# Kernel tuning notes

Hardware: AMD Instinct MI355X
Metric: run time of the kernel (lower is better)

## Reference

```python
import jax, jax.numpy as jnp
from jax import lax
import numpy as np

B = 16
E, NH, FF, L = 768, 12, 3072, 8
D = E // NH  # 64, per-head dim
PATCH_DIM = 16 * 16 * 16  # 4096


def setup_inputs() -> dict:
    key = jax.random.key(0)
    ks = jax.random.split(key, 16)
    s = 0.02
    def n(k, shape):
        return jax.random.normal(k, shape, dtype=jnp.float32) * s
    return {
        "x": jax.random.normal(ks[0], (B, 512, 512, 3), dtype=jnp.float32),
        "conv1_w": n(ks[1], (3, 3, 3, 16)), "conv1_b": jnp.zeros((16,), jnp.float32),
        "conv2_w": n(ks[2], (3, 3, 16, 16)), "conv2_b": jnp.zeros((16,), jnp.float32),
        "proj_w": n(ks[3], (PATCH_DIM, E)), "proj_b": jnp.zeros((E,), jnp.float32),
        "Wq": n(ks[4], (L, E, E)), "bq": jnp.zeros((L, E), jnp.float32),
        "Wk": n(ks[5], (L, E, E)), "bk": jnp.zeros((L, E), jnp.float32),
        "Wv": n(ks[6], (L, E, E)), "bv": jnp.zeros((L, E), jnp.float32),
        "Wo": n(ks[7], (L, E, E)), "bo": jnp.zeros((L, E), jnp.float32),
        "W1": n(ks[8], (L, E, FF)), "b1": jnp.zeros((L, FF), jnp.float32),
        "W2": n(ks[9], (L, FF, E)), "b2": jnp.zeros((L, E), jnp.float32),
        "ln1_g": jnp.ones((L, E), jnp.float32), "ln1_b": jnp.zeros((L, E), jnp.float32),
        "ln2_g": jnp.ones((L, E), jnp.float32), "ln2_b": jnp.zeros((L, E), jnp.float32),
        "head_w": n(ks[10], (E, 1)), "head_b": jnp.zeros((1,), jnp.float32),
    }


def _ln(x, g, b, eps=1e-6):
    m = jnp.mean(x, axis=-1, keepdims=True)
    v = jnp.var(x, axis=-1, keepdims=True)
    return (x - m) * lax.rsqrt(v + eps) * g + b


def _forward(x, conv1_w, conv1_b, conv2_w, conv2_b, proj_w, proj_b,
             Wq, bq, Wk, bk, Wv, bv, Wo, bo, W1, b1, W2, b2,
             ln1_g, ln1_b, ln2_g, ln2_b, head_w, head_b):
    dn = ('NHWC', 'HWIO', 'NHWC')
    h = jax.nn.relu(lax.conv_general_dilated(x, conv1_w, (1, 1), 'VALID', dimension_numbers=dn) + conv1_b)
    h = lax.reduce_window(h, -jnp.inf, lax.max, (1, 2, 2, 1), (1, 2, 2, 1), 'VALID')  # (B,255,255,16)
    h = jax.nn.relu(lax.conv_general_dilated(h, conv2_w, (1, 1), 'VALID', dimension_numbers=dn) + conv2_b)
    h = lax.reduce_window(h, -jnp.inf, lax.max, (1, 2, 2, 1), (1, 2, 2, 1), 'VALID')  # (B,126,126,16)
    # tf.image.extract_patches 16x16 stride 16 SAME: pad 126 -> 128 (1 before, 1 after)
    h = jnp.pad(h, ((0, 0), (1, 1), (1, 1), (0, 0)))
    Bc = h.shape[0]
    patches = h.reshape(Bc, 8, 16, 8, 16, 16).transpose(0, 1, 3, 2, 4, 5).reshape(Bc, 64, PATCH_DIM)
    t = patches @ proj_w + proj_b  # (B,64,768)
    scale = 1.0 / jnp.sqrt(jnp.float32(D))  # tf code scales by sqrt(per-head key dim)
    for i in range(L):
        q = (t @ Wq[i] + bq[i]).reshape(Bc, -1, NH, D).transpose(0, 2, 1, 3)
        k = (t @ Wk[i] + bk[i]).reshape(Bc, -1, NH, D).transpose(0, 2, 1, 3)
        v = (t @ Wv[i] + bv[i]).reshape(Bc, -1, NH, D).transpose(0, 2, 1, 3)
        w = jax.nn.softmax(jnp.einsum('bhqd,bhkd->bhqk', q, k) * scale, axis=-1)
        a = jnp.einsum('bhqk,bhkd->bhqd', w, v)  # (B,H,S,D)
        # FAITHFUL to original: reshape (B,H,S,D) -> (B,S,E) directly (no transpose back)
        a = a.reshape(Bc, -1, E)
        a = a @ Wo[i] + bo[i]
        o1 = _ln(t + a, ln1_g[i], ln1_b[i])
        f = jax.nn.relu(o1 @ W1[i] + b1[i]) @ W2[i] + b2[i]
        t = _ln(o1 + f, ln2_g[i], ln2_b[i])
    pooled = jnp.mean(t, axis=1)  # GlobalAveragePooling1D
    return jax.nn.sigmoid(pooled @ head_w + head_b)


def reference(x, conv1_w, conv1_b, conv2_w, conv2_b, proj_w, proj_b,
              Wq, bq, Wk, bk, Wv, bv, Wo, bo, W1, b1, W2, b2,
              ln1_g, ln1_b, ln2_g, ln2_b, head_w, head_b):
    return _forward(x, conv1_w, conv1_b, conv2_w, conv2_b, proj_w, proj_b,
                    Wq, bq, Wk, bk, Wv, bv, Wo, bo, W1, b1, W2, b2,
                    ln1_g, ln1_b, ln2_g, ln2_b, head_w, head_b)
```

## Files before the change

### kernel.cpp

```cpp
#include <hip/hip_runtime.h>
#include <hip/hip_bf16.h>
#include <cstdint>
#include <cstddef>

typedef __bf16 bf16;
typedef __attribute__((ext_vector_type(8))) __bf16 bf16x8;
typedef __attribute__((ext_vector_type(4))) float f32x4;

__global__ __launch_bounds__(256) void wtrans(const float* __restrict__ src,
    bf16* __restrict__ dst, int K, int N) {
  __shared__ float tile[32][33];
  int l = blockIdx.z;
  src += (size_t)l * K * N; dst += (size_t)l * K * N;
  int n0 = blockIdx.x * 32, k0 = blockIdx.y * 32;
  int tx = threadIdx.x & 31, ty = threadIdx.x >> 5;
#pragma unroll
  for (int i = 0; i < 4; i++) {
    int k = ty + i * 8;
    tile[k][tx] = src[(size_t)(k0 + k) * N + n0 + tx];
  }
  __syncthreads();
#pragma unroll
  for (int i = 0; i < 4; i++) {
    int n = ty + i * 8;
    dst[(size_t)(n0 + n) * K + k0 + tx] = (bf16)tile[tx][n];
  }
}

__global__ __launch_bounds__(256) void conv1_pool(const float* __restrict__ x,
    const float* __restrict__ w, const float* __restrict__ bias,
    bf16* __restrict__ out) {
  __shared__ float ws[432];
  __shared__ float bs[16];
  int t = threadIdx.x;
  for (int i = t; i < 432; i += 256) ws[i] = w[i];
  if (t < 16) bs[t] = bias[t];
  __syncthreads();
  int idx = blockIdx.x * 256 + t;
  if (idx >= 16 * 255 * 255) return;
  int xo = idx % 255; int tmp = idx / 255; int yo = tmp % 255; int b = tmp / 255;
  float best[16];
#pragma unroll
  for (int c = 0; c < 16; c++) best[c] = 0.f;
#pragma unroll
  for (int py = 0; py < 2; py++)
#pragma unroll
  for (int px = 0; px < 2; px++) {
    float acc[16];
#pragma unroll
    for (int c = 0; c < 16; c++) acc[c] = bs[c];
    int iy0 = yo * 2 + py, ix0 = xo * 2 + px;
    for (int ky = 0; ky < 3; ky++)
    for (int kx = 0; kx < 3; kx++) {
      const float* xp = x + ((size_t)(b * 512 + iy0 + ky) * 512 + (ix0 + kx)) * 3;
      float v0 = xp[0], v1 = xp[1], v2 = xp[2];
      const float* wp = &ws[((ky * 3 + kx) * 3) * 16];
#pragma unroll
      for (int c = 0; c < 16; c++) acc[c] = fmaf(v0, wp[c], acc[c]);
#pragma unroll
      for (int c = 0; c < 16; c++) acc[c] = fmaf(v1, wp[16 + c], acc[c]);
#pragma unroll
      for (int c = 0; c < 16; c++) acc[c] = fmaf(v2, wp[32 + c], acc[c]);
    }
#pragma unroll
    for (int c = 0; c < 16; c++) best[c] = fmaxf(best[c], acc[c]);
  }
  bf16* op = out + (size_t)idx * 16;
#pragma unroll
  for (int c = 0; c < 16; c++) op[c] = (bf16)best[c];
}

__global__ __launch_bounds__(256) void conv2_mfma(const bf16* __restrict__ in,
    const float* __restrict__ w, const float* __restrict__ bias,
    bf16* __restrict__ patches) {
  __shared__ alignas(16) bf16 xlo[1156 * 8];
  __shared__ alignas(16) bf16 xhi[1156 * 8];
  __shared__ float ws[2304];
  int t = threadIdx.x;
  int tx = blockIdx.x, ty = blockIdx.y, b = blockIdx.z;
  for (int i = t; i < 2304; i += 256) ws[i] = w[i];
  int r0 = 32 * ty - 2, c0 = 32 * tx - 2;
  for (int i = t; i < 1156; i += 256) {
    int rr = i / 34, cc = i % 34;
    int gr = min(max(r0 + rr, 0), 254), gc = min(max(c0 + cc, 0), 254);
    const bf16* ip = in + ((size_t)(b * 255 + gr) * 255 + gc) * 16;
    *(uint4*)&xlo[i * 8] = *(const uint4*)ip;
    *(uint4*)&xhi[i * 8] = *(const uint4*)(ip + 8);
  }
  __syncthreads();
  int lane = t & 63, wave = t >> 6;
  int lr = lane & 15, lq = lane >> 4;
  int tapsel = lq >> 1;
  int ci0 = (lq & 1) * 8;
  bf16x8 bfrag[5];
  int koff[5];
#pragma unroll
  for (int c2 = 0; c2 < 5; c2++) {
    int tap = 2 * c2 + tapsel;
    bf16x8 v;
#pragma unroll
    for (int j = 0; j < 8; j++)
      v[j] = (tap < 9) ? (bf16)ws[tap * 256 + (ci0 + j) * 16 + lr] : (bf16)0.f;
    bfrag[c2] = v;
    int tc = min(tap, 8);
    koff[c2] = (tc / 3) * 34 + (tc % 3);
  }
  const bf16* plane = (lq & 1) ? xhi : xlo;
  float bco = bias[lr];
  bf16* pout = patches + ((size_t)(b * 64 + ty * 8 + tx) * 4096);
#pragma unroll
  for (int yy = 0; yy < 4; yy++) {
    int Y = wave * 4 + yy;
    int yp = ty * 16 + Y;
    bool padrow = (yp == 0 || yp == 127);
#pragma unroll
    for (int hx = 0; hx < 2; hx++) {
      f32x4 a0 = {0.f, 0.f, 0.f, 0.f}, a1 = {0.f, 0.f, 0.f, 0.f};
      int base0 = (2 * Y) * 34 + hx * 16 + lr;
      int base1 = base0 + 34;
#pragma unroll
      for (int c2 = 0; c2 < 5; c2++) {
        bf16x8 f0 = *(const bf16x8*)&plane[(base0 + koff[c2]) * 8];
        a0 = __builtin_amdgcn_mfma_f32_16x16x32_bf16(f0, bfrag[c2], a0, 0, 0, 0);
      }
#pragma unroll
      for (int c2 = 0; c2 < 5; c2++) {
        bf16x8 f1 = *(const bf16x8*)&plane[(base1 + koff[c2]) * 8];
        a1 = __builtin_amdgcn_mfma_f32_16x16x32_bf16(f1, bfrag[c2], a1, 0, 0, 0);
      }
      float m0 = fmaxf(fmaxf(a0[0], a0[1]), fmaxf(a1[0], a1[1]));
      float m1 = fmaxf(fmaxf(a0[2], a0[3]), fmaxf(a1[2], a1[3]));
      m0 = fmaxf(m0 + bco, 0.f);
      m1 = fmaxf(m1 + bco, 0.f);
      int px0 = hx * 8 + 2 * lq, px1 = px0 + 1;
      int xp0 = tx * 16 + px0, xp1 = xp0 + 1;
      if (padrow || xp0 == 0) m0 = 0.f;
      if (padrow || xp1 == 127) m1 = 0.f;
      pout[Y * 256 + px0 * 16 + lr] = (bf16)m0;
      pout[Y * 256 + px1 * 16 + lr] = (bf16)m1;
    }
  }
}

#define LSTR 72

template<int MODE>
__device__ __forceinline__ void gemm_core(const bf16* __restrict__ A,
    const bf16* __restrict__ Bt, const float* __restrict__ bias,
    float* __restrict__ Cf, bf16* __restrict__ Cb,
    int bm, int bn, int N, int K, int k0, int kc) {
  __shared__ alignas(16) bf16 As[64 * LSTR];
  __shared__ alignas(16) bf16 Bs[64 * LSTR];
  int t = threadIdx.x, lane = t & 63, wave = t >> 6;
  int wm = (wave >> 1) * 32, wn = (wave & 1) * 32;
  int lq = lane >> 4, lr = lane & 15;
  f32x4 acc[2][2];
#pragma unroll
  for (int i = 0; i < 2; i++)
#pragma unroll
  for (int j = 0; j < 2; j++) acc[i][j] = (f32x4){0.f, 0.f, 0.f, 0.f};
  int r = t >> 2, c = (t & 3) * 16;
  const bf16* Ap = A + (size_t)(bm + r) * K + k0 + c;
  const bf16* Bp = Bt + (size_t)(bn + r) * K + k0 + c;
  bf16* AsW = &As[r * LSTR + c];
  bf16* BsW = &Bs[r * LSTR + c];
  uint4 a0 = *(const uint4*)Ap, a1 = *(const uint4*)(Ap + 8);
  uint4 b0 = *(const uint4*)Bp, b1 = *(const uint4*)(Bp + 8);
  for (int kk = 64; kk <= kc; kk += 64) {
    *(uint4*)AsW = a0; *(uint4*)(AsW + 8) = a1;
    *(uint4*)BsW = b0; *(uint4*)(BsW + 8) = b1;
    __syncthreads();
    if (kk < kc) {
      Ap += 64; Bp += 64;
      a0 = *(const uint4*)Ap; a1 = *(const uint4*)(Ap + 8);
      b0 = *(const uint4*)Bp; b1 = *(const uint4*)(Bp + 8);
    }
#pragma unroll
    for (int ks = 0; ks < 2; ks++) {
      bf16x8 af0 = *(const bf16x8*)&As[(wm + lr) * LSTR + ks * 32 + lq * 8];
      bf16x8 af1 = *(const bf16x8*)&As[(wm + 16 + lr) * LSTR + ks * 32 + lq * 8];
      bf16x8 bfr0 = *(const bf16x8*)&Bs[(wn + lr) * LSTR + ks * 32 + lq * 8];
      bf16x8 bfr1 = *(const bf16x8*)&Bs[(wn + 16 + lr) * LSTR + ks * 32 + lq * 8];
      acc[0][0] = __builtin_amdgcn_mfma_f32_16x16x32_bf16(af0, bfr0, acc[0][0], 0, 0, 0);
      acc[0][1] = __builtin_amdgcn_mfma_f32_16x16x32_bf16(af0, bfr1, acc[0][1], 0, 0, 0);
      acc[1][0] = __builtin_amdgcn_mfma_f32_16x16x32_bf16(af1, bfr0, acc[1][0], 0, 0, 0);
      acc[1][1] = __builtin_amdgcn_mfma_f32_16x16x32_bf16(af1, bfr1, acc[1][1], 0, 0, 0);
    }
    __syncthreads();
  }
#pragma unroll
  for (int mi = 0; mi < 2; mi++)
#pragma unroll
  for (int ni = 0; ni < 2; ni++) {
    int col = bn + wn + ni * 16 + lr;
#pragma unroll
    for (int rr = 0; rr < 4; rr++) {
      int row = bm + wm + mi * 16 + lq * 4 + rr;
      float v = acc[mi][ni][rr];
      if (MODE == 1) {
        v = fmaxf(v + bias[col], 0.f);
        Cb[(size_t)row * N + col] = (bf16)v;
      } else {
        Cf[(size_t)row * N + col] = v;
      }
    }
  }
}

template<int MODE>
__global__ __launch_bounds__(256) void gemm_std(const bf16* __restrict__ A,
    const bf16* __restrict__ Bt, const float* __restrict__ bias,
    float* __restrict__ Cf, bf16* __restrict__ Cb, int N, int K, int KC) {
  int s = blockIdx.z;
  float* Cfp = Cf ? Cf + (size_t)s * 1024 * N : nullptr;
  gemm_core<MODE>(A, Bt, bias, Cfp, Cb, blockIdx.y * 64, blockIdx.x * 64, N, K, s * KC, KC);
}

__global__ __launch_bounds__(256) void gemm_qkv(const bf16* __restrict__ A,
    const bf16* __restrict__ Btq, const bf16* __restrict__ Btk, const bf16* __restrict__ Btv,
    float* __restrict__ qp, float* __restrict__ kp, float* __restrict__ vp) {
  int z = blockIdx.z;
  int sel = z >> 1, s = z & 1;
  const bf16* Bt = (sel == 0) ? Btq : (sel == 1) ? Btk : Btv;
  float* C = ((sel == 0) ? qp : (sel == 1) ? kp : vp) + (size_t)s * 786432;
  gemm_core<0>(A, Bt, nullptr, C, nullptr, blockIdx.y * 64, blockIdx.x * 64, 768, 768, s * 384, 384);
}

__global__ __launch_bounds__(256) void attn_kernel(const float* __restrict__ Qp,
    const float* __restrict__ Kp, const float* __restrict__ Vp,
    const float* __restrict__ bq, const float* __restrict__ bk, const float* __restrict__ bv,
    bf16* __restrict__ Aout) {
  __shared__ alignas(16) float qs[64 * 68];
  __shared__ alignas(16) float ks[64 * 68];
  __shared__ alignas(16) float ss[64 * 68];
  int t = threadIdx.x;
  int bh = blockIdx.x; int b = bh / 12, h = bh % 12;
  size_t base = (size_t)b * 49152 + h * 64;
  const float* qb0 = Qp + base; const float* qb1 = qb0 + 786432;
  const float* kb0 = Kp + base; const float* kb1 = kb0 + 786432;
  const float* vb0 = Vp + base; const float* vb1 = vb0 + 786432;
  {
    int s = t >> 2, qd = (t & 3) * 16;
#pragma unroll
    for (int j = 0; j < 16; j += 4) {
      float4 q0 = *(const float4*)(qb0 + (size_t)s * 768 + qd + j);
      float4 q1 = *(const float4*)(qb1 + (size_t)s * 768 + qd + j);
      float4 qb4 = *(const float4*)(bq + h * 64 + qd + j);
      float4 k0 = *(const float4*)(kb0 + (size_t)s * 768 + qd + j);
      float4 k1 = *(const float4*)(kb1 + (size_t)s * 768 + qd + j);
      float4 kb4 = *(const float4*)(bk + h * 64 + qd + j);
      qs[s * 68 + qd + j + 0] = q0.x + q1.x + qb4.x;
      qs[s * 68 + qd + j + 1] = q0.y + q1.y + qb4.y;
      qs[s * 68 + qd + j + 2] = q0.z + q1.z + qb4.z;
      qs[s * 68 + qd + j + 3] = q0.w + q1.w + qb4.w;
      ks[s * 68 + qd + j + 0] = k0.x + k1.x + kb4.x;
      ks[s * 68 + qd + j + 1] = k0.y + k1.y + kb4.y;
      ks[s * 68 + qd + j + 2] = k0.z + k1.z + kb4.z;
      ks[s * 68 + qd + j + 3] = k0.w + k1.w + kb4.w;
    }
  }
  __syncthreads();
  int r = t >> 4, c = t & 15;
  {
    float sc[4][4];
#pragma unroll
    for (int i = 0; i < 4; i++)
#pragma unroll
    for (int j = 0; j < 4; j++) sc[i][j] = 0.f;
    for (int k = 0; k < 64; k += 4) {
      float4 qv[4], kv[4];
#pragma unroll
      for (int i = 0; i < 4; i++) qv[i] = *(const float4*)&qs[(r + 16 * i) * 68 + k];
#pragma unroll
      for (int j = 0; j < 4; j++) kv[j] = *(const float4*)&ks[(c + 16 * j) * 68 + k];
#pragma unroll
      for (int i = 0; i < 4; i++)
#pragma unroll
      for (int j = 0; j < 4; j++)
        sc[i][j] += qv[i].x * kv[j].x + qv[i].y * kv[j].y + qv[i].z * kv[j].z + qv[i].w * kv[j].w;
    }
#pragma unroll
    for (int i = 0; i < 4; i++)
#pragma unroll
    for (int j = 0; j < 4; j++)
      ss[(r + 16 * i) * 68 + c + 16 * j] = sc[i][j] * 0.125f;
  }
  __syncthreads();
  {
    int d = t & 63, s0 = (t >> 6) * 16;
    float bvd = bv[h * 64 + d];
    alignas(16) float vv[16];
#pragma unroll
    for (int i = 0; i < 16; i++)
      vv[i] = vb0[(size_t)(s0 + i) * 768 + d] + vb1[(size_t)(s0 + i) * 768 + d] + bvd;
#pragma unroll
    for (int i = 0; i < 16; i += 4) *(float4*)&qs[d * 68 + s0 + i] = *(float4*)&vv[i];
  }
  {
    int lane = t & 63, wave = t >> 6;
    for (int rr = 0; rr < 16; rr++) {
      int row = wave * 16 + rr;
      float v = ss[row * 68 + lane];
      float m = v;
#pragma unroll
      for (int off = 32; off > 0; off >>= 1) m = fmaxf(m, __shfl_xor(m, off));
      float e = __expf(v - m);
      float ssum = e;
#pragma unroll
      for (int off = 32; off > 0; off >>= 1) ssum += __shfl_xor(ssum, off);
      ss[row * 68 + lane] = e / ssum;
    }
  }
  __syncthreads();
  {
    float oc[4][4];
#pragma unroll
    for (int i = 0; i < 4; i++)
#pragma unroll
    for (int j = 0; j < 4; j++) oc[i][j] = 0.f;
    for (int k = 0; k < 64; k += 4) {
      float4 pv[4], vv[4];
#pragma unroll
      for (int i = 0; i < 4; i++) pv[i] = *(const float4*)&ss[(r + 16 * i) * 68 + k];
#pragma unroll
      for (int j = 0; j < 4; j++) vv[j] = *(const float4*)&qs[(c + 16 * j) * 68 + k];
#pragma unroll
      for (int i = 0; i < 4; i++)
#pragma unroll
      for (int j = 0; j < 4; j++)
        oc[i][j] += pv[i].x * vv[j].x + pv[i].y * vv[j].y + pv[i].z * vv[j].z + pv[i].w * vv[j].w;
    }
    bf16* ob = Aout + (size_t)b * 49152 + h * 4096;
#pragma unroll
    for (int i = 0; i < 4; i++)
#pragma unroll
    for (int j = 0; j < 4; j++)
      ob[(r + 16 * i) * 64 + c + 16 * j] = (bf16)oc[i][j];
  }
}

template<int S>
__global__ __launch_bounds__(256) void ln_kernel(const float* __restrict__ X,
    const float* __restrict__ Y, const float* __restrict__ yb,
    const float* __restrict__ g, const float* __restrict__ bta,
    float* __restrict__ Of, bf16* __restrict__ Ob) {
  int row = blockIdx.x, t = threadIdx.x;
  const float* xp = X + (size_t)row * 768;
  float vals[3]; float s = 0.f, s2 = 0.f;
#pragma unroll
  for (int i = 0; i < 3; i++) {
    int e = t + 256 * i;
    float v = xp[e] + yb[e];
#pragma unroll
    for (int p = 0; p < S; p++) v += Y[(size_t)p * 786432 + (size_t)row * 768 + e];
    vals[i] = v; s += v; s2 = fmaf(v, v, s2);
  }
#pragma unroll
  for (int off = 32; off > 0; off >>= 1) { s += __shfl_xor(s, off); s2 += __shfl_xor(s2, off); }
  __shared__ float rs[4], rs2[4];
  if ((t & 63) == 0) { rs[t >> 6] = s; rs2[t >> 6] = s2; }
  __syncthreads();
  s = rs[0] + rs[1] + rs[2] + rs[3];
  s2 = rs2[0] + rs2[1] + rs2[2] + rs2[3];
  float mean = s * (1.f / 768.f);
  float var = s2 * (1.f / 768.f) - mean * mean;
  float rstd = rsqrtf(var + 1e-6f);
  float* ofp = Of + (size_t)row * 768;
  bf16* obp = Ob + (size_t)row * 768;
#pragma unroll
  for (int i = 0; i < 3; i++) {
    int e = t + 256 * i;
    float o = (vals[i] - mean) * rstd * g[e] + bta[e];
    ofp[e] = o; obp[e] = (bf16)o;
  }
}

__global__ __launch_bounds__(256) void reduce2(const float* __restrict__ P,
    const float* __restrict__ bias, float* __restrict__ Of, bf16* __restrict__ Ob) {
  int row = blockIdx.x, t = threadIdx.x;
#pragma unroll
  for (int i = 0; i < 3; i++) {
    int e = t + 256 * i;
    float v = P[(size_t)row * 768 + e] + P[786432 + (size_t)row * 768 + e] + bias[e];
    Of[(size_t)row * 768 + e] = v;
    Ob[(size_t)row * 768 + e] = (bf16)v;
  }
}

__global__ __launch_bounds__(256) void head_kernel(const float* __restrict__ T,
    const float* __restrict__ hw, const float* __restrict__ hbp, float* __restrict__ out) {
  int b = blockIdx.x, t = threadIdx.x;
  float acc = 0.f;
#pragma unroll
  for (int i = 0; i < 3; i++) {
    int e = t + 256 * i;
    float s = 0.f;
    for (int si = 0; si < 64; si++) s += T[(size_t)(b * 64 + si) * 768 + e];
    acc = fmaf(s * (1.f / 64.f), hw[e], acc);
  }
#pragma unroll
  for (int off = 32; off > 0; off >>= 1) acc += __shfl_xor(acc, off);
  __shared__ float rs[4];
  if ((t & 63) == 0) rs[t >> 6] = acc;
  __syncthreads();
  if (t == 0) {
    float z = rs[0] + rs[1] + rs[2] + rs[3] + hbp[0];
    out[b] = 1.f / (1.f + expf(-z));
  }
}

extern "C" void kernel_launch(void* const* d_in, const int* in_sizes, int n_in,
                              void* d_out, int out_size, void* d_ws, size_t ws_size,
                              hipStream_t stream) {
  const float* x     = (const float*)d_in[0];
  const float* c1w   = (const float*)d_in[1];
  const float* c1b   = (const float*)d_in[2];
  const float* c2w   = (const float*)d_in[3];
  const float* c2b   = (const float*)d_in[4];
  const float* projw = (const float*)d_in[5];
  const float* projb = (const float*)d_in[6];
  const float* Wq    = (const float*)d_in[7];
  const float* bq    = (const float*)d_in[8];
  const float* Wk    = (const float*)d_in[9];
  const float* bk    = (const float*)d_in[10];
  const float* Wv    = (const float*)d_in[11];
  const float* bv    = (const float*)d_in[12];
  const float* Wo    = (const float*)d_in[13];
  const float* bo    = (const float*)d_in[14];
  const float* W1    = (const float*)d_in[15];
  const float* b1    = (const float*)d_in[16];
  const float* W2    = (const float*)d_in[17];
  const float* b2    = (const float*)d_in[18];
  const float* ln1g  = (const float*)d_in[19];
  const float* ln1b  = (const float*)d_in[20];
  const float* ln2g  = (const float*)d_in[21];
  const float* ln2b  = (const float*)d_in[22];
  const float* headw = (const float*)d_in[23];
  const float* headb = (const float*)d_in[24];
  float* out = (float*)d_out;

  char* wp = (char*)d_ws;
  auto alloc = [&](size_t bytes) { char* p = wp; wp += (bytes + 255) & ~(size_t)255; return p; };
  bf16* c1p     = (bf16*)alloc((size_t)16 * 255 * 255 * 16 * 2);
  bf16* patches = (bf16*)alloc((size_t)1024 * 4096 * 2);
  bf16* projT   = (bf16*)alloc((size_t)4096 * 768 * 2);
  bf16* WqT     = (bf16*)alloc((size_t)8 * 768 * 768 * 2);
  bf16* WkT     = (bf16*)alloc((size_t)8 * 768 * 768 * 2);
  bf16* WvT     = (bf16*)alloc((size_t)8 * 768 * 768 * 2);
  bf16* WoT     = (bf16*)alloc((size_t)8 * 768 * 768 * 2);
  bf16* W1T     = (bf16*)alloc((size_t)8 * 768 * 3072 * 2);
  bf16* W2T     = (bf16*)alloc((size_t)8 * 3072 * 768 * 2);
  float* pp     = (float*)alloc((size_t)2 * 1024 * 768 * 4);
  float* tf     = (float*)alloc((size_t)1024 * 768 * 4);
  bf16*  tb     = (bf16*)alloc((size_t)1024 * 768 * 2);
  float* qp     = (float*)alloc((size_t)2 * 1024 * 768 * 4);
  float* kp     = (float*)alloc((size_t)2 * 1024 * 768 * 4);
  float* vp     = (float*)alloc((size_t)2 * 1024 * 768 * 4);
  float* wop    = (float*)alloc((size_t)2 * 1024 * 768 * 4);
  float* w2p    = (float*)alloc((size_t)4 * 1024 * 768 * 4);
  bf16*  ab     = (bf16*)alloc((size_t)1024 * 768 * 2);
  float* o1f    = (float*)alloc((size_t)1024 * 768 * 4);
  bf16*  o1b    = (bf16*)alloc((size_t)1024 * 768 * 2);
  bf16*  hbuf   = (bf16*)alloc((size_t)1024 * 3072 * 2);

  wtrans<<<dim3(24, 128, 1), 256, 0, stream>>>(projw, projT, 4096, 768);
  wtrans<<<dim3(24, 24, 8), 256, 0, stream>>>(Wq, WqT, 768, 768);
  wtrans<<<dim3(24, 24, 8), 256, 0, stream>>>(Wk, WkT, 768, 768);
  wtrans<<<dim3(24, 24, 8), 256, 0, stream>>>(Wv, WvT, 768, 768);
  wtrans<<<dim3(24, 24, 8), 256, 0, stream>>>(Wo, WoT, 768, 768);
  wtrans<<<dim3(96, 24, 8), 256, 0, stream>>>(W1, W1T, 768, 3072);
  wtrans<<<dim3(24, 96, 8), 256, 0, stream>>>(W2, W2T, 3072, 768);

  conv1_pool<<<4065, 256, 0, stream>>>(x, c1w, c1b, c1p);
  conv2_mfma<<<dim3(8, 8, 16), 256, 0, stream>>>(c1p, c2w, c2b, patches);
  gemm_std<0><<<dim3(12, 16, 2), 256, 0, stream>>>(patches, projT, nullptr, pp, nullptr, 768, 4096, 2048);
  reduce2<<<1024, 256, 0, stream>>>(pp, projb, tf, tb);

  for (int i = 0; i < 8; i++) {
    gemm_qkv<<<dim3(12, 16, 6), 256, 0, stream>>>(tb,
        WqT + (size_t)i * 589824, WkT + (size_t)i * 589824, WvT + (size_t)i * 589824,
        qp, kp, vp);
    attn_kernel<<<192, 256, 0, stream>>>(qp, kp, vp,
        bq + i * 768, bk + i * 768, bv + i * 768, ab);
    gemm_std<0><<<dim3(12, 16, 2), 256, 0, stream>>>(ab, WoT + (size_t)i * 589824,
        nullptr, wop, nullptr, 768, 768, 384);
    ln_kernel<2><<<1024, 256, 0, stream>>>(tf, wop, bo + i * 768,
        ln1g + i * 768, ln1b + i * 768, o1f, o1b);
    gemm_std<1><<<dim3(48, 16, 1), 256, 0, stream>>>(o1b, W1T + (size_t)i * 2359296,
        b1 + i * 3072, nullptr, hbuf, 3072, 768, 768);
    gemm_std<0><<<dim3(12, 16, 4), 256, 0, stream>>>(hbuf, W2T + (size_t)i * 2359296,
        nullptr, w2p, nullptr, 768, 3072, 768);
    ln_kernel<4><<<1024, 256, 0, stream>>>(o1f, w2p, b2 + i * 768,
        ln2g + i * 768, ln2b + i * 768, tf, tb);
  }
  head_kernel<<<16, 256, 0, stream>>>(tf, headw, headb, out);
}
```

Before: 1.055 ms.

## Rewrite conv1+pool as tiled MFMA kernel with shared-memory input staging

Replaces the scalar per-pixel FMA conv1+maxpool kernel with a tiled version. It stages a 34x35 input patch in shared memory as bf16 (channels padded to 8) and computes the 3x3x3 convolution with bf16 16x16x32 MFMA instructions, one per kernel row. The 2x2 max, bias and ReLU are done in registers. The aim is to remove redundant global loads and cut FP32 FMA work. In exchange, inputs and weights are rounded to bf16 (a precision risk), most MFMA K lanes are wasted on zero padding, and the output stores are scattered.

```diff
diff --git a/kernel.cpp b/kernel.cpp
--- a/kernel.cpp
+++ b/kernel.cpp
@@ -27,47 +27,65 @@
   }
 }
 
-__global__ __launch_bounds__(256) void conv1_pool(const float* __restrict__ x,
+__global__ __launch_bounds__(256) void conv1_mfma(const float* __restrict__ x,
     const float* __restrict__ w, const float* __restrict__ bias,
     bf16* __restrict__ out) {
-  __shared__ float ws[432];
-  __shared__ float bs[16];
+  __shared__ alignas(16) bf16 xs[34 * 35 * 8];
   int t = threadIdx.x;
-  for (int i = t; i < 432; i += 256) ws[i] = w[i];
-  if (t < 16) bs[t] = bias[t];
-  __syncthreads();
-  int idx = blockIdx.x * 256 + t;
-  if (idx >= 16 * 255 * 255) return;
-  int xo = idx % 255; int tmp = idx / 255; int yo = tmp % 255; int b = tmp / 255;
-  float best[16];
-#pragma unroll
-  for (int c = 0; c < 16; c++) best[c] = 0.f;
-#pragma unroll
-  for (int py = 0; py < 2; py++)
-#pragma unroll
-  for (int px = 0; px < 2; px++) {
-    float acc[16];
-#pragma unroll
-    for (int c = 0; c < 16; c++) acc[c] = bs[c];
-    int iy0 = yo * 2 + py, ix0 = xo * 2 + px;
-    for (int ky = 0; ky < 3; ky++)
-    for (int kx = 0; kx < 3; kx++) {
-      const float* xp = x + ((size_t)(b * 512 + iy0 + ky) * 512 + (ix0 + kx)) * 3;
-      float v0 = xp[0], v1 = xp[1], v2 = xp[2];
-      const float* wp = &ws[((ky * 3 + kx) * 3) * 16];
-#pragma unroll
-      for (int c = 0; c < 16; c++) acc[c] = fmaf(v0, wp[c], acc[c]);
-#pragma unroll
-      for (int c = 0; c < 16; c++) acc[c] = fmaf(v1, wp[16 + c], acc[c]);
-#pragma unroll
-      for (int c = 0; c < 16; c++) acc[c] = fmaf(v2, wp[32 + c], acc[c]);
-    }
-#pragma unroll
-    for (int c = 0; c < 16; c++) best[c] = fmaxf(best[c], acc[c]);
-  }
-  bf16* op = out + (size_t)idx * 16;
-#pragma unroll
-  for (int c = 0; c < 16; c++) op[c] = (bf16)best[c];
+  int bx = blockIdx.x, by = blockIdx.y, b = blockIdx.z;
+  int r0 = 32 * by, c0 = 32 * bx;
+  for (int i = t; i < 34 * 35; i += 256) {
+    int rr = i / 35, cc = i % 35;
+    int gr = min(r0 + rr, 511), gc = min(c0 + cc, 511);
+    const float* ip = x + ((size_t)(b * 512 + gr) * 512 + gc) * 3;
+    bf16x8 pv = {(bf16)ip[0], (bf16)ip[1], (bf16)ip[2],
+                 (bf16)0.f, (bf16)0.f, (bf16)0.f, (bf16)0.f, (bf16)0.f};
+    *(bf16x8*)&xs[i * 8] = pv;
+  }
+  int lane = t & 63, wave = t >> 6;
+  int lr = lane & 15, lq = lane >> 4;
+  bf16x8 bfrag[3];
+#pragma unroll
+  for (int ky = 0; ky < 3; ky++) {
+    bf16x8 v;
+#pragma unroll
+    for (int j = 0; j < 8; j++)
+      v[j] = (lq < 3 && j < 3) ? (bf16)w[((ky * 3 + lq) * 3 + j) * 16 + lr] : (bf16)0.f;
+    bfrag[ky] = v;
+  }
+  float bco = bias[lr];
+  __syncthreads();
+#pragma unroll
+  for (int yy = 0; yy < 4; yy++) {
+    int Y = wave * 4 + yy;
+    int yp = by * 16 + Y;
+    int cy = 2 * Y;
+#pragma unroll
+    for (int hx = 0; hx < 2; hx++) {
+      f32x4 a0 = {0.f, 0.f, 0.f, 0.f}, a1 = {0.f, 0.f, 0.f, 0.f};
+      int pbase = hx * 16 + lr + lq;
+#pragma unroll
+      for (int ky = 0; ky < 3; ky++) {
+        bf16x8 f0 = *(const bf16x8*)&xs[((cy + ky) * 35 + pbase) * 8];
+        a0 = __builtin_amdgcn_mfma_f32_16x16x32_bf16(f0, bfrag[ky], a0, 0, 0, 0);
+      }
+#pragma unroll
+      for (int ky = 0; ky < 3; ky++) {
+        bf16x8 f1 = *(const bf16x8*)&xs[((cy + 1 + ky) * 35 + pbase) * 8];
+        a1 = __builtin_amdgcn_mfma_f32_16x16x32_bf16(f1, bfrag[ky], a1, 0, 0, 0);
+      }
+      float m0 = fmaxf(fmaxf(a0[0], a0[1]), fmaxf(a1[0], a1[1]));
+      float m1 = fmaxf(fmaxf(a0[2], a0[3]), fmaxf(a1[2], a1[3]));
+      m0 = fmaxf(m0 + bco, 0.f);
+      m1 = fmaxf(m1 + bco, 0.f);
+      int xp0 = bx * 16 + hx * 8 + 2 * lq, xp1 = xp0 + 1;
+      if (yp < 255) {
+        bf16* op = out + ((size_t)(b * 255 + yp) * 255) * 16 + lr;
+        if (xp0 < 255) op[xp0 * 16] = (bf16)m0;
+        if (xp1 < 255) op[xp1 * 16] = (bf16)m1;
+      }
+    }
+  }
 }
 
 __global__ __launch_bounds__(256) void conv2_mfma(const bf16* __restrict__ in,
@@ -471,7 +489,7 @@
   wtrans<<<dim3(96, 24, 8), 256, 0, stream>>>(W1, W1T, 768, 3072);
   wtrans<<<dim3(24, 96, 8), 256, 0, stream>>>(W2, W2T, 3072, 768);
 
-  conv1_pool<<<4065, 256, 0, stream>>>(x, c1w, c1b, c1p);
+  conv1_mfma<<<dim3(16, 16, 16), 256, 0, stream>>>(x, c1w, c1b, c1p);
   conv2_mfma<<<dim3(8, 8, 16), 256, 0, stream>>>(c1p, c2w, c2b, patches);
   gemm_std<0><<<dim3(12, 16, 2), 256, 0, stream>>>(patches, projT, nullptr, pp, nullptr, 768, 4096, 2048);
   reduce2<<<1024, 256, 0, stream>>>(pp, projb, tf, tb);
```

Result: faster. 995.5 us (-5.6%).
